# Kernel tuning notes

Hardware: AMD Instinct MI355X
Metric: run time of the kernel (lower is better)

## Reference

```python
import jax, jax.numpy as jnp
import numpy as np

# Faithful translations of the torch lambdas:
# r0: identity; r90: transpose(-2,-1); r180: flip(-2); r270: transpose(-2,-1) then flip(-1)
_r0 = lambda xi: xi
_r90 = lambda xi: jnp.swapaxes(xi, -2, -1)
_r180 = lambda xi: jnp.flip(xi, axis=-2)
_r270 = lambda xi: jnp.flip(jnp.swapaxes(xi, -2, -1), axis=-1)


def setup_inputs() -> dict:
    key = jax.random.key(0)
    kx, kl = jax.random.split(key)
    B, C, H, W = 256, 3, 224, 224  # square spatial required by transpose-in-place semantics
    x = jax.random.normal(kx, (B, C, H, W), dtype=jnp.float32)
    label = jax.random.randint(kl, (B,), 0, 4, dtype=jnp.int32)
    return {"x": x, "label": label}


def reference(x, label):
    # Single fused per-sample-indexed rotation via vmap + lax.switch —
    # replaces the python loop / per-sample kernel launches of the original.
    def rotate_one(xi, li):
        return jax.lax.switch(li, [_r0, _r90, _r180, _r270], xi)

    out = jax.vmap(rotate_one)(x, label)
    return (out, label)
```

## Files before the change

### kernel.cpp

```cpp
#include <hip/hip_runtime.h>


#define HW 224
#define W4 56
#define TILE 32
#define NT 7

typedef float f4 __attribute__((ext_vector_type(4)));

__global__ __launch_bounds__(256) void rot4_kernel(const float* __restrict__ x,
                                                   const int* __restrict__ label,
                                                   float* __restrict__ out,
                                                   float* __restrict__ out_label,
                                                   int B) {
    const int t = threadIdx.x;

    {
        int li = blockIdx.x * 256 + t;
        if (blockIdx.x < (B + 255) / 256 && li < B) out_label[li] = (float)label[li];
    }

    int blk = blockIdx.x;
    const int th = blk % NT; blk /= NT;
    const int c  = blk % 3;  blk /= 3;
    const int b  = blk;

    const int lab = label[b];
    const size_t plane = (size_t)(b * 3 + c) * (HW * HW);
    const float*  in = x + plane;
    float*        o  = out + plane;
    const f4* in4 = (const f4*)in;
    f4*       o4  = (f4*)o;
    const int h0 = th * TILE;

    if (lab == 0) {
        const size_t base = (size_t)h0 * W4;
        #pragma unroll
        for (int k = 0; k < NT; ++k) {
            size_t i = base + (size_t)k * 256 + t;
            f4 v = __builtin_nontemporal_load(in4 + i);
            __builtin_nontemporal_store(v, o4 + i);
        }
    } else if (lab == 2) {
        #pragma unroll
        for (int k = 0; k < NT; ++k) {
            int idx = k * 256 + t;
            int rr  = idx / W4;
            int cc  = idx - rr * W4;
            size_t src = (size_t)(HW - 1 - (h0 + rr)) * W4 + cc;
            size_t dst = (size_t)(h0 + rr) * W4 + cc;
            f4 v = __builtin_nontemporal_load(in4 + src);
            __builtin_nontemporal_store(v, o4 + dst);
        }
    } else {
        __shared__ float tb[2][TILE][TILE + 1];
        const int r  = t >> 3;
        const int c4 = t & 7;

        auto src_ptr = [&](int tw) {
            const int w0 = tw * TILE;
            const int rbase = (lab == 1) ? w0 : (HW - TILE - w0);
            return (const f4*)(in + (size_t)(rbase + r) * HW + h0 + c4 * 4);
        };

        f4 v[NT];
        #pragma unroll
        for (int k = 0; k < NT; ++k)
            v[k] = __builtin_nontemporal_load(src_ptr(k));

        #pragma unroll
        for (int tw = 0; tw < NT; ++tw) {
            float (*tbuf)[TILE + 1] = tb[tw & 1];
            tbuf[r][c4 * 4 + 0] = v[tw].x;
            tbuf[r][c4 * 4 + 1] = v[tw].y;
            tbuf[r][c4 * 4 + 2] = v[tw].z;
            tbuf[r][c4 * 4 + 3] = v[tw].w;
            __syncthreads();
            f4 w;
            if (lab == 1) {
                w.x = tbuf[c4 * 4 + 0][r];
                w.y = tbuf[c4 * 4 + 1][r];
                w.z = tbuf[c4 * 4 + 2][r];
                w.w = tbuf[c4 * 4 + 3][r];
            } else {
                w.x = tbuf[31 - (c4 * 4 + 0)][r];
                w.y = tbuf[31 - (c4 * 4 + 1)][r];
                w.z = tbuf[31 - (c4 * 4 + 2)][r];
                w.w = tbuf[31 - (c4 * 4 + 3)][r];
            }
            const int w0 = tw * TILE;
            __builtin_nontemporal_store(
                w, (f4*)(o + (size_t)(h0 + r) * HW + w0 + c4 * 4));
        }
    }
}

extern "C" void kernel_launch(void* const* d_in, const int* in_sizes, int n_in,
                              void* d_out, int out_size, void* d_ws, size_t ws_size,
                              hipStream_t stream) {
    const float* x     = (const float*)d_in[0];
    const int*   label = (const int*)d_in[1];
    float*       out   = (float*)d_out;

    const int B = in_sizes[1];
    const int nblocks = B * 3 * NT;
    const size_t img_elems = (size_t)B * 3 * HW * HW;

    rot4_kernel<<<nblocks, 256, 0, stream>>>(x, label, out, out + img_elems, B);
}
```

Measured before the change: 250.2 us.

## Transpose rotations through single 112x112 shared tile per block quadrant

Reorganizes the work so each block handles one quadrant (112x112) of a plane with 448 threads, instead of a 32-row strip split into seven 32x32 transposes with a sync per tile. For the 90/270 cases the whole quadrant is staged in about 50KB of LDS and written out after a single barrier. Label conversion moves to block 0 only. This cuts barriers and block count, but the large LDS footprint lowers occupancy and the LDS writes are strided.

```diff
diff --git a/kernel.cpp b/kernel.cpp
--- a/kernel.cpp
+++ b/kernel.cpp
@@ -3,94 +3,97 @@
 
 #define HW 224
 #define W4 56
-#define TILE 32
-#define NT 7
+#define TS 112
+#define TQ4 28
+#define LS 113
 
 typedef float f4 __attribute__((ext_vector_type(4)));
 
-__global__ __launch_bounds__(256) void rot4_kernel(const float* __restrict__ x,
+__global__ __launch_bounds__(448) void rot4_kernel(const float* __restrict__ x,
                                                    const int* __restrict__ label,
                                                    float* __restrict__ out,
                                                    float* __restrict__ out_label,
                                                    int B) {
     const int t = threadIdx.x;
 
-    {
-        int li = blockIdx.x * 256 + t;
-        if (blockIdx.x < (B + 255) / 256 && li < B) out_label[li] = (float)label[li];
-    }
+    if (blockIdx.x == 0)
+        for (int li = t; li < B; li += 448) out_label[li] = (float)label[li];
 
     int blk = blockIdx.x;
-    const int th = blk % NT; blk /= NT;
-    const int c  = blk % 3;  blk /= 3;
-    const int b  = blk;
+    const int q = blk & 3;  blk >>= 2;
+    const int c = blk % 3;
+    const int b = blk / 3;
 
     const int lab = label[b];
     const size_t plane = (size_t)(b * 3 + c) * (HW * HW);
-    const float*  in = x + plane;
-    float*        o  = out + plane;
-    const f4* in4 = (const f4*)in;
-    f4*       o4  = (f4*)o;
-    const int h0 = th * TILE;
+    const float* in = x + plane;
+    float*       o  = out + plane;
 
     if (lab == 0) {
-        const size_t base = (size_t)h0 * W4;
+        const f4* in4 = (const f4*)in;
+        f4*       o4  = (f4*)o;
+        const int base = q * 3136;
         #pragma unroll
-        for (int k = 0; k < NT; ++k) {
-            size_t i = base + (size_t)k * 256 + t;
+        for (int k = 0; k < 7; ++k) {
+            int i = base + k * 448 + t;
             f4 v = __builtin_nontemporal_load(in4 + i);
             __builtin_nontemporal_store(v, o4 + i);
         }
     } else if (lab == 2) {
+        const f4* in4 = (const f4*)in;
+        f4*       o4  = (f4*)o;
         #pragma unroll
-        for (int k = 0; k < NT; ++k) {
-            int idx = k * 256 + t;
+        for (int k = 0; k < 7; ++k) {
+            int idx = k * 448 + t;
             int rr  = idx / W4;
             int cc  = idx - rr * W4;
-            size_t src = (size_t)(HW - 1 - (h0 + rr)) * W4 + cc;
-            size_t dst = (size_t)(h0 + rr) * W4 + cc;
-            f4 v = __builtin_nontemporal_load(in4 + src);
-            __builtin_nontemporal_store(v, o4 + dst);
+            int row = q * W4 + rr;
+            f4 v = __builtin_nontemporal_load(in4 + (size_t)(HW - 1 - row) * W4 + cc);
+            __builtin_nontemporal_store(v, o4 + (size_t)row * W4 + cc);
         }
     } else {
-        __shared__ float tb[2][TILE][TILE + 1];
-        const int r  = t >> 3;
-        const int c4 = t & 7;
+        __shared__ float trans[TS * LS];
+        const int g  = t / TQ4;
+        const int cq = t % TQ4;
+        const int Ti = q >> 1, Tj = q & 1;
+        const int Ri = Ti * TS, Cj = Tj * TS;
+        const int SR = (lab == 1) ? Cj : (TS - Cj);
+        const int SC = Ri;
 
-        auto src_ptr = [&](int tw) {
-            const int w0 = tw * TILE;
-            const int rbase = (lab == 1) ? w0 : (HW - TILE - w0);
-            return (const f4*)(in + (size_t)(rbase + r) * HW + h0 + c4 * 4);
-        };
-
-        f4 v[NT];
+        f4 v[7];
         #pragma unroll
-        for (int k = 0; k < NT; ++k)
-            v[k] = __builtin_nontemporal_load(src_ptr(k));
-
+        for (int p = 0; p < 7; ++p) {
+            int s = p * 16 + g;
+            v[p] = __builtin_nontemporal_load(
+                (const f4*)(in + (size_t)(SR + s) * HW + SC + cq * 4));
+        }
         #pragma unroll
-        for (int tw = 0; tw < NT; ++tw) {
-            float (*tbuf)[TILE + 1] = tb[tw & 1];
-            tbuf[r][c4 * 4 + 0] = v[tw].x;
-            tbuf[r][c4 * 4 + 1] = v[tw].y;
-            tbuf[r][c4 * 4 + 2] = v[tw].z;
-            tbuf[r][c4 * 4 + 3] = v[tw].w;
-            __syncthreads();
+        for (int p = 0; p < 7; ++p) {
+            int s = p * 16 + g;
+            trans[(cq * 4 + 0) * LS + s] = v[p].x;
+            trans[(cq * 4 + 1) * LS + s] = v[p].y;
+            trans[(cq * 4 + 2) * LS + s] = v[p].z;
+            trans[(cq * 4 + 3) * LS + s] = v[p].w;
+        }
+        __syncthreads();
+        #pragma unroll
+        for (int p = 0; p < 7; ++p) {
+            int r = p * 16 + g;
+            const float* tr = &trans[r * LS];
             f4 w;
             if (lab == 1) {
-                w.x = tbuf[c4 * 4 + 0][r];
-                w.y = tbuf[c4 * 4 + 1][r];
-                w.z = tbuf[c4 * 4 + 2][r];
-                w.w = tbuf[c4 * 4 + 3][r];
+                w.x = tr[cq * 4 + 0];
+                w.y = tr[cq * 4 + 1];
+                w.z = tr[cq * 4 + 2];
+                w.w = tr[cq * 4 + 3];
             } else {
-                w.x = tbuf[31 - (c4 * 4 + 0)][r];
-                w.y = tbuf[31 - (c4 * 4 + 1)][r];
-                w.z = tbuf[31 - (c4 * 4 + 2)][r];
-                w.w = tbuf[31 - (c4 * 4 + 3)][r];
+                w.x = tr[111 - (cq * 4 + 0)];
+                w.y = tr[111 - (cq * 4 + 1)];
+                w.z = tr[111 - (cq * 4 + 2)];
+                w.w = tr[111 - (cq * 4 + 3)];
             }
-            const int w0 = tw * TILE;
             __builtin_nontemporal_store(
-                w, (f4*)(o + (size_t)(h0 + r) * HW + w0 + c4 * 4));
+                w, (f4*)(o + (size_t)(Ri + r) * HW + Cj + cq * 4));
         }
     }
 }
@@ -103,8 +106,8 @@
     float*       out   = (float*)d_out;
 
     const int B = in_sizes[1];
-    const int nblocks = B * 3 * NT;
+    const int nblocks = B * 3 * 4;
     const size_t img_elems = (size_t)B * 3 * HW * HW;
 
-    rot4_kernel<<<nblocks, 256, 0, stream>>>(x, label, out, out + img_elems, B);
+    rot4_kernel<<<nblocks, 448, 0, stream>>>(x, label, out, out + img_elems, B);
 }
```

Measured after the change: 256.3 us. 2.5% more time.
